# Optimization experiments

Measured on AMD Instinct MI355X. Metric: run time of the kernel, lower is better.

Reference implementation:

```python
import jax, jax.numpy as jnp
import numpy as np

CHUNK_SIZE = 64
EPS = 1e-6


def setup_inputs() -> dict:
    key = jax.random.key(0)
    ks = jax.random.split(key, 5)
    B, NH, S, DH = 2, 16, 4096, 64
    return {
        "q": jax.random.normal(ks[0], (B, NH, S, DH), dtype=jnp.float32),
        "k": jax.random.normal(ks[1], (B, NH, S, DH), dtype=jnp.float32),
        "v": jax.random.normal(ks[2], (B, NH, S, DH), dtype=jnp.float32),
        "igate_preact": jax.random.normal(ks[3], (B, NH, S), dtype=jnp.float32),
        "fgate_preact": jax.random.normal(ks[4], (B, NH, S), dtype=jnp.float32),
    }


def _mlstm_intra(q, k, v, ig, fg, chunk_size, eps):
    # q,k,v: [B,NH,S,DH]; ig,fg: [B,NH,S]
    B, NH, S, DH = q.shape
    L = chunk_size
    NC = S // L
    qc = q.reshape(B, NH, NC, L, DH)
    kc = k.reshape(B, NH, NC, L, DH)
    vc = v.reshape(B, NH, NC, L, DH)
    igc = ig.reshape(B, NH, NC, L)
    fgc = fg.reshape(B, NH, NC, L)

    # log forget gates and their within-chunk cumulative sums
    log_fg = jax.nn.log_sigmoid(fgc)                      # [B,NH,NC,L]
    log_fg_cum = jnp.cumsum(log_fg, axis=-1)              # [B,NH,NC,L]

    # gated decay matrix: logD[i,j] = sum_{t=j+1..i} log f_t + i_j  for j<=i
    log_fg_mat = log_fg_cum[..., :, None] - log_fg_cum[..., None, :]  # [B,NH,NC,L,L]
    log_D = log_fg_mat + igc[..., None, :]
    causal = jnp.tril(jnp.ones((L, L), dtype=bool))
    log_D = jnp.where(causal, log_D, -jnp.inf)

    # stabilizer (row-wise max)
    m = jnp.max(log_D, axis=-1)                           # [B,NH,NC,L]
    D = jnp.exp(log_D - m[..., None])                     # [B,NH,NC,L,L]

    # QK scores scaled, gated by decay matrix
    scale = 1.0 / jnp.sqrt(jnp.asarray(DH, dtype=q.dtype))
    scores = jnp.einsum("bncld,bncsd->bncls", qc, kc) * scale
    C = scores * D                                        # [B,NH,NC,L,L]

    # stabilized normalizer: max(|row sum|, exp(-m))
    n = jnp.maximum(jnp.abs(jnp.sum(C, axis=-1)), jnp.exp(-m))  # [B,NH,NC,L]
    h = jnp.einsum("bncls,bncsd->bncld", C, vc) / (n[..., None] + eps)
    return h.reshape(B, NH, S, DH)


def reference(q, k, v, igate_preact, fgate_preact):
    return _mlstm_intra(q, k, v, igate_preact, fgate_preact, CHUNK_SIZE, EPS)
```

## Files before the change

### kernel.cpp

```cpp
#include <hip/hip_runtime.h>
#include <hip/hip_bf16.h>
#include <math.h>

namespace {

typedef __bf16 bf16x8 __attribute__((ext_vector_type(8)));
typedef float f32x4 __attribute__((ext_vector_type(4)));

constexpr int L = 64;
constexpr int DH = 64;

__device__ __forceinline__ int kkey(int r) { return (r ^ (r >> 2)) & 7; }
__device__ __forceinline__ int swz(int row, int col) {
  return row * 128 + ((((col >> 3) ^ kkey(row)) & 7) << 4) + (col & 7) * 2;
}

__device__ __forceinline__ unsigned short bfbits(float f) {
  __bf16 h = (__bf16)f;
  return __builtin_bit_cast(unsigned short, h);
}
__device__ __forceinline__ __bf16 tobf(float f) { return (__bf16)f; }
__device__ __forceinline__ unsigned long long pack4(float a, float b, float c,
                                                    float d) {
  return (unsigned long long)bfbits(a) | ((unsigned long long)bfbits(b) << 16) |
         ((unsigned long long)bfbits(c) << 32) |
         ((unsigned long long)bfbits(d) << 48);
}

__global__ __launch_bounds__(64, 2) void mlstm_mfma(
    const float* __restrict__ q, const float* __restrict__ k,
    const float* __restrict__ v, const float* __restrict__ ig,
    const float* __restrict__ fg, float* __restrict__ out) {

  __shared__ __align__(16) char qs_raw[64 * 128];
  __shared__ __align__(16) char vt_raw[64 * 128];
  __shared__ __align__(16) float ea_sh[64];
  __shared__ float eb_sh[64], em_sh[64];

  const int lane = threadIdx.x;
  const int m = lane & 15;
  const int g = lane >> 4;
  const size_t cbase = (size_t)blockIdx.x * (L * DH);
  const size_t gb = (size_t)blockIdx.x * L;

  const float fgv = fg[gb + lane];
  const float igv = ig[gb + lane];

  const float4* v4 = (const float4*)(v + cbase);
  const float4* q4 = (const float4*)(q + cbase);
  float4 vbuf[16], qraw[16];
#pragma unroll
  for (int it = 0; it < 16; ++it) vbuf[it] = v4[it * 64 + lane];
#pragma unroll
  for (int it = 0; it < 16; ++it) qraw[it] = q4[it * 64 + lane];

  float4 kbuf[4][2][2];
#pragma unroll
  for (int rb = 0; rb < 4; ++rb)
#pragma unroll
    for (int kb = 0; kb < 2; ++kb) {
      const int off = (rb * 16 + m) * 64 + kb * 32 + g * 8;
      kbuf[rb][kb][0] = *(const float4*)(k + cbase + off);
      kbuf[rb][kb][1] = *(const float4*)(k + cbase + off + 4);
    }

  {
    const float lf = fminf(fgv, 0.f) - log1pf(__expf(-fabsf(fgv)));
    float cum = lf;
#pragma unroll
    for (int o = 1; o < 64; o <<= 1) {
      const float t = __shfl_up(cum, o, 64);
      if (lane >= o) cum += t;
    }
    const float a = igv - cum;
    float b = a;
#pragma unroll
    for (int o = 1; o < 64; o <<= 1) {
      const float t = __shfl_up(b, o, 64);
      if (lane >= o) b = fmaxf(b, t);
    }
    const float bmax = __shfl(b, 63, 64);
    ea_sh[lane] = 0.125f * __expf(a - bmax);
    eb_sh[lane] = __expf(bmax - b);
    em_sh[lane] = __expf(-(b + cum));
  }

  {
    unsigned short* vt = (unsigned short*)vt_raw;
#pragma unroll
    for (int it = 0; it < 16; ++it) {
      const int idx = it * 64 + lane;
      const int j = idx >> 4;
      const int d0 = (idx & 15) * 4;
      vt[swz(d0 + 0, j) >> 1] = bfbits(vbuf[it].x);
      vt[swz(d0 + 1, j) >> 1] = bfbits(vbuf[it].y);
      vt[swz(d0 + 2, j) >> 1] = bfbits(vbuf[it].z);
      vt[swz(d0 + 3, j) >> 1] = bfbits(vbuf[it].w);
    }
  }

#pragma unroll
  for (int it = 0; it < 16; ++it) {
    const int idx = it * 64 + lane;
    const int row = idx >> 4;
    const int col = (idx & 15) * 4;
    *(unsigned long long*)(qs_raw + swz(row, col)) =
        pack4(qraw[it].x, qraw[it].y, qraw[it].z, qraw[it].w);
  }

  bf16x8 kf[4][2];
#pragma unroll
  for (int rb = 0; rb < 4; ++rb)
#pragma unroll
    for (int kb = 0; kb < 2; ++kb) {
      const float4 k0 = kbuf[rb][kb][0], k1 = kbuf[rb][kb][1];
      kf[rb][kb] = bf16x8{tobf(k0.x), tobf(k0.y), tobf(k0.z), tobf(k0.w),
                          tobf(k1.x), tobf(k1.y), tobf(k1.z), tobf(k1.w)};
    }

  bf16x8 qf[4][2];
#pragma unroll
  for (int cb = 0; cb < 4; ++cb)
#pragma unroll
    for (int kb = 0; kb < 2; ++kb)
      qf[cb][kb] =
          *(const bf16x8*)(qs_raw + swz(cb * 16 + m, kb * 32 + g * 8));

  bf16x8 vfr[4][2];
#pragma unroll
  for (int db = 0; db < 4; ++db)
#pragma unroll
    for (int jb = 0; jb < 2; ++jb)
      vfr[db][jb] =
          *(const bf16x8*)(vt_raw + swz(db * 16 + m, jb * 32 + g * 8));

  f32x4 st[4][4];
#pragma unroll
  for (int cb = 0; cb < 4; ++cb)
#pragma unroll
    for (int rb = 0; rb < 4; ++rb) {
      if (rb > cb) continue;
      f32x4 acc = {0.f, 0.f, 0.f, 0.f};
      acc = __builtin_amdgcn_mfma_f32_16x16x32_bf16(kf[rb][0], qf[cb][0], acc, 0, 0, 0);
      acc = __builtin_amdgcn_mfma_f32_16x16x32_bf16(kf[rb][1], qf[cb][1], acc, 0, 0, 0);
      st[rb][cb] = acc;
    }

  float ea_j[4][4];
#pragma unroll
  for (int rb = 0; rb < 4; ++rb) {
    const float4 ea4 = *(const float4*)&ea_sh[rb * 16 + g * 4];
    ea_j[rb][0] = ea4.x; ea_j[rb][1] = ea4.y;
    ea_j[rb][2] = ea4.z; ea_j[rb][3] = ea4.w;
  }

  float invr[4];
#pragma unroll
  for (int cb = 0; cb < 4; ++cb) {
    const int i = cb * 16 + m;
    const float ebv = eb_sh[i];
    float rs = 0.f;
    const int rbfill = cb | 1;
#pragma unroll
    for (int rb = 0; rb < 4; ++rb) {
      if (rb > rbfill) continue;
      unsigned long long wp = 0ull;
      if (rb <= cb) {
        float vv[4];
#pragma unroll
        for (int e = 0; e < 4; ++e) {
          const int j = rb * 16 + g * 4 + e;
          vv[e] = (j <= i) ? st[rb][cb][e] * ea_j[rb][e] * ebv : 0.f;
          rs += vv[e];
        }
        wp = pack4(vv[0], vv[1], vv[2], vv[3]);
      }
      *(unsigned long long*)(qs_raw + swz(i, rb * 16 + g * 4)) = wp;
    }
    rs += __shfl_xor(rs, 16, 64);
    rs += __shfl_xor(rs, 32, 64);
    const float n = fmaxf(fabsf(rs), em_sh[i]);
    invr[cb] = 1.f / (n + 1e-6f);
  }

#pragma unroll
  for (int ib = 0; ib < 4; ++ib) {
    const int i = ib * 16 + m;
    const bf16x8 c0 = *(const bf16x8*)(qs_raw + swz(i, g * 8));
    f32x4 acc[4];
#pragma unroll
    for (int db = 0; db < 4; ++db) {
      f32x4 z = {0.f, 0.f, 0.f, 0.f};
      acc[db] = __builtin_amdgcn_mfma_f32_16x16x32_bf16(vfr[db][0], c0, z, 0, 0, 0);
    }
    if (ib >= 2) {
      const bf16x8 c1 = *(const bf16x8*)(qs_raw + swz(i, 32 + g * 8));
#pragma unroll
      for (int db = 0; db < 4; ++db)
        acc[db] = __builtin_amdgcn_mfma_f32_16x16x32_bf16(vfr[db][1], c1, acc[db], 0, 0, 0);
    }
    const float iv = invr[ib];
    float* op = out + cbase + i * 64 + g * 4;
#pragma unroll
    for (int db = 0; db < 4; ++db) {
      const f32x4 hv = acc[db];
      *(float4*)(op + db * 16) =
          make_float4(hv[0] * iv, hv[1] * iv, hv[2] * iv, hv[3] * iv);
    }
  }
}

}

extern "C" void kernel_launch(void* const* d_in, const int* in_sizes, int n_in,
                              void* d_out, int out_size, void* d_ws,
                              size_t ws_size, hipStream_t stream) {
  const float* q = (const float*)d_in[0];
  const float* k = (const float*)d_in[1];
  const float* v = (const float*)d_in[2];
  const float* ig = (const float*)d_in[3];
  const float* fg = (const float*)d_in[4];
  float* out = (float*)d_out;

  const int total = in_sizes[0];
  const int nchunks = total / (L * DH);
  mlstm_mfma<<<dim3(nchunks), dim3(64), 0, stream>>>(q, k, v, ig, fg, out);
}
```

Before: 26.94 us.

## Load Q and K directly into LDS via global_load_lds with swizzled layout

After: 34.01 us. 1.26x slower.

```diff
diff --git a/kernel.cpp b/kernel.cpp
--- a/kernel.cpp
+++ b/kernel.cpp
@@ -1,6 +1,7 @@
 #include <hip/hip_runtime.h>
 #include <hip/hip_bf16.h>
 #include <math.h>
+#include <stdint.h>
 
 namespace {
 
@@ -27,13 +28,21 @@
          ((unsigned long long)bfbits(d) << 48);
 }
 
-__global__ __launch_bounds__(64, 2) void mlstm_mfma(
+__device__ __forceinline__ void gload16(const float* gsrc, float* ldst) {
+  __builtin_amdgcn_global_load_lds(
+      (const __attribute__((address_space(1))) uint32_t*)gsrc,
+      (__attribute__((address_space(3))) uint32_t*)ldst, 16, 0, 0);
+}
+
+__global__ __launch_bounds__(64, 1) void mlstm_mfma(
     const float* __restrict__ q, const float* __restrict__ k,
     const float* __restrict__ v, const float* __restrict__ ig,
     const float* __restrict__ fg, float* __restrict__ out) {
 
-  __shared__ __align__(16) char qs_raw[64 * 128];
+  __shared__ __align__(16) float q_lds[64 * 64];
+  __shared__ __align__(16) float k_lds[64 * 64];
   __shared__ __align__(16) char vt_raw[64 * 128];
+  __shared__ __align__(16) char cs_raw[64 * 128];
   __shared__ __align__(16) float ea_sh[64];
   __shared__ float eb_sh[64], em_sh[64];
 
@@ -47,22 +56,21 @@
   const float igv = ig[gb + lane];
 
   const float4* v4 = (const float4*)(v + cbase);
-  const float4* q4 = (const float4*)(q + cbase);
-  float4 vbuf[16], qraw[16];
+  float4 vbuf[16];
 #pragma unroll
   for (int it = 0; it < 16; ++it) vbuf[it] = v4[it * 64 + lane];
-#pragma unroll
-  for (int it = 0; it < 16; ++it) qraw[it] = q4[it * 64 + lane];
-
-  float4 kbuf[4][2][2];
-#pragma unroll
-  for (int rb = 0; rb < 4; ++rb)
-#pragma unroll
-    for (int kb = 0; kb < 2; ++kb) {
-      const int off = (rb * 16 + m) * 64 + kb * 32 + g * 8;
-      kbuf[rb][kb][0] = *(const float4*)(k + cbase + off);
-      kbuf[rb][kb][1] = *(const float4*)(k + cbase + off + 4);
-    }
+
+  {
+    const int rsub = lane >> 4;
+    const int slot = lane & 15;
+#pragma unroll
+    for (int it = 0; it < 16; ++it) {
+      const int r = it * 4 + rsub;
+      const int coff = r * 64 + ((slot ^ kkey(r)) << 2);
+      gload16(q + cbase + coff, &q_lds[it * 256]);
+      gload16(k + cbase + coff, &k_lds[it * 256]);
+    }
+  }
 
   {
     const float lf = fminf(fgv, 0.f) - log1pf(__expf(-fabsf(fgv)));
@@ -99,32 +107,26 @@
     }
   }
 
-#pragma unroll
-  for (int it = 0; it < 16; ++it) {
-    const int idx = it * 64 + lane;
-    const int row = idx >> 4;
-    const int col = (idx & 15) * 4;
-    *(unsigned long long*)(qs_raw + swz(row, col)) =
-        pack4(qraw[it].x, qraw[it].y, qraw[it].z, qraw[it].w);
-  }
-
-  bf16x8 kf[4][2];
+  asm volatile("s_waitcnt vmcnt(0)" ::: "memory");
+
+  bf16x8 qf[4][2], kf[4][2];
 #pragma unroll
   for (int rb = 0; rb < 4; ++rb)
 #pragma unroll
     for (int kb = 0; kb < 2; ++kb) {
-      const float4 k0 = kbuf[rb][kb][0], k1 = kbuf[rb][kb][1];
-      kf[rb][kb] = bf16x8{tobf(k0.x), tobf(k0.y), tobf(k0.z), tobf(k0.w),
-                          tobf(k1.x), tobf(k1.y), tobf(k1.z), tobf(k1.w)};
-    }
-
-  bf16x8 qf[4][2];
-#pragma unroll
-  for (int cb = 0; cb < 4; ++cb)
-#pragma unroll
-    for (int kb = 0; kb < 2; ++kb)
-      qf[cb][kb] =
-          *(const bf16x8*)(qs_raw + swz(cb * 16 + m, kb * 32 + g * 8));
+      const int row = rb * 16 + m;
+      const int c4 = kb * 8 + g * 2;
+      const int o0 = row * 64 + (((c4 + 0) ^ kkey(row)) << 2);
+      const int o1 = row * 64 + (((c4 + 1) ^ kkey(row)) << 2);
+      const f32x4 ka = *(const f32x4*)&k_lds[o0];
+      const f32x4 kb4 = *(const f32x4*)&k_lds[o1];
+      const f32x4 qa = *(const f32x4*)&q_lds[o0];
+      const f32x4 qb = *(const f32x4*)&q_lds[o1];
+      kf[rb][kb] = bf16x8{tobf(ka[0]), tobf(ka[1]), tobf(ka[2]), tobf(ka[3]),
+                          tobf(kb4[0]), tobf(kb4[1]), tobf(kb4[2]), tobf(kb4[3])};
+      qf[rb][kb] = bf16x8{tobf(qa[0]), tobf(qa[1]), tobf(qa[2]), tobf(qa[3]),
+                          tobf(qb[0]), tobf(qb[1]), tobf(qb[2]), tobf(qb[3])};
+    }
 
   bf16x8 vfr[4][2];
 #pragma unroll
@@ -175,7 +177,7 @@
         }
         wp = pack4(vv[0], vv[1], vv[2], vv[3]);
       }
-      *(unsigned long long*)(qs_raw + swz(i, rb * 16 + g * 4)) = wp;
+      *(unsigned long long*)(cs_raw + swz(i, rb * 16 + g * 4)) = wp;
     }
     rs += __shfl_xor(rs, 16, 64);
     rs += __shfl_xor(rs, 32, 64);
@@ -186,7 +188,7 @@
 #pragma unroll
   for (int ib = 0; ib < 4; ++ib) {
     const int i = ib * 16 + m;
-    const bf16x8 c0 = *(const bf16x8*)(qs_raw + swz(i, g * 8));
+    const bf16x8 c0 = *(const bf16x8*)(cs_raw + swz(i, g * 8));
     f32x4 acc[4];
 #pragma unroll
     for (int db = 0; db < 4; ++db) {
@@ -194,7 +196,7 @@
       acc[db] = __builtin_amdgcn_mfma_f32_16x16x32_bf16(vfr[db][0], c0, z, 0, 0, 0);
     }
     if (ib >= 2) {
-      const bf16x8 c1 = *(const bf16x8*)(qs_raw + swz(i, 32 + g * 8));
+      const bf16x8 c1 = *(const bf16x8*)(cs_raw + swz(i, 32 + g * 8));
 #pragma unroll
       for (int db = 0; db < 4; ++db)
         acc[db] = __builtin_amdgcn_mfma_f32_16x16x32_bf16(vfr[db][1], c1, acc[db], 0, 0, 0);
```
